# Performance work log

Measured on AMD Instinct MI355X. Metric: run time of the kernel, lower is better.

Reference implementation:

```python
import jax, jax.numpy as jnp
import numpy as np

WS = 7        # window size
NH = 8        # num heads


def setup_inputs() -> dict:
    key = jax.random.key(0)
    ks = jax.random.split(key, 5)
    B, N, C = 32, 3136, 512
    x = jax.random.normal(ks[0], (B, N, C), dtype=jnp.float32)
    s = 1.0 / np.sqrt(C)
    w_qkv = jax.random.normal(ks[1], (C, 3 * C), dtype=jnp.float32) * s
    b_qkv = jax.random.normal(ks[2], (3 * C,), dtype=jnp.float32) * 0.01
    w_proj = jax.random.normal(ks[3], (C, C), dtype=jnp.float32) * s
    b_proj = jax.random.normal(ks[4], (C,), dtype=jnp.float32) * 0.01
    return {"x": x, "w_qkv": w_qkv, "b_qkv": b_qkv, "w_proj": w_proj, "b_proj": b_proj}


def reference(x, w_qkv, b_qkv, w_proj, b_proj):
    B, N, C = x.shape
    H = W = int(round(N ** 0.5))
    hd = C // NH
    t = WS * WS  # 49 tokens per window
    # window partition: (B,N,C) -> (nW, 49, C)
    xw = x.reshape(B, H // WS, WS, W // WS, WS, C)
    xw = jnp.transpose(xw, (0, 1, 3, 2, 4, 5)).reshape(-1, t, C)
    # qkv projection; NOTE: no head permute (faithful to source), so
    # q,k,v : (nW, 49, NH, hd)
    qkv = (xw @ w_qkv + b_qkv).reshape(-1, t, 3, NH, hd)
    q, k, v = qkv[:, :, 0], qkv[:, :, 1], qkv[:, :, 2]
    # q @ k^T contracts head_dim, attends over heads axis: (nW, 49, NH, NH)
    attn = jnp.einsum('wthd,wtgd->wthg', q, k) * (hd ** -0.5)
    attn = jax.nn.softmax(attn, axis=-1)
    out = jnp.einsum('wthg,wtgd->wthd', attn, v)          # (nW, 49, NH, hd)
    # faithful transpose(1,2).reshape(-1, 49, C) (scrambles layout, as in torch)
    out = jnp.transpose(out, (0, 2, 1, 3)).reshape(-1, t, C)
    out = out @ w_proj + b_proj
    # window merge back to (B, N, C)
    out = out.reshape(B, H // WS, W // WS, WS, WS, C)
    out = jnp.transpose(out, (0, 1, 3, 2, 4, 5)).reshape(B, N, C)
    return out
```

## Files before the change

### kernel.cpp

```cpp
#include <hip/hip_runtime.h>
#include <stdint.h>
#include <stddef.h>

typedef short s16;
typedef __attribute__((ext_vector_type(8))) short short8;
typedef __attribute__((ext_vector_type(4))) float floatx4;

__device__ __forceinline__ float bf2f(short s) {
    union { float f; uint32_t u; } c; c.u = ((uint32_t)(uint16_t)s) << 16; return c.f;
}
__device__ __forceinline__ short f2bf(float f) {
    union { float f; uint32_t u; } c; c.f = f;
    uint32_t u = c.u;
    u += 0x7fffu + ((u >> 16) & 1u);
    return (short)(u >> 16);
}

__global__ __launch_bounds__(256) void cvt_kernel(const float* __restrict__ src,
                                                  s16* __restrict__ dst) {
    size_t i = (size_t)blockIdx.x * 256 + threadIdx.x;
    const floatx4* s4 = (const floatx4*)src;
    floatx4 a = s4[i * 2], b = s4[i * 2 + 1];
    short8 o;
    o[0] = f2bf(a[0]); o[1] = f2bf(a[1]); o[2] = f2bf(a[2]); o[3] = f2bf(a[3]);
    o[4] = f2bf(b[0]); o[5] = f2bf(b[1]); o[6] = f2bf(b[2]); o[7] = f2bf(b[3]);
    ((short8*)dst)[i] = o;
}

__global__ __launch_bounds__(256) void transpose_kernel(const float* __restrict__ w,
                                                        s16* __restrict__ wt,
                                                        int K, int N) {
    int idx = blockIdx.x * 256 + threadIdx.x;
    if (idx >= K * N) return;
    int n = idx / K, k = idx - n * K;
    wt[idx] = f2bf(w[(size_t)k * N + n]);
}

__device__ __forceinline__ const s16* x_row_ptr(const s16* xb, int m) {
    int win = m / 49, t = m - win * 49;
    int b = win >> 6, rem = win & 63, hb = rem >> 3, wb = rem & 7;
    int r = t / 7, c = t - r * 7;
    int n = (hb * 7 + r) * 56 + wb * 7 + c;
    return xb + ((size_t)b * 3136 + n) * 512;
}

template <int MODE>
__global__ __launch_bounds__(256) void gemm_kernel(const s16* __restrict__ A,
                                                   const s16* __restrict__ Bt,
                                                   const float* __restrict__ bias,
                                                   void* __restrict__ outp) {
    constexpr int NT = (MODE == 0) ? 12 : 4;
    const int tm = blockIdx.x / NT, tn = blockIdx.x % NT;
    const int tid = threadIdx.x, wave = tid >> 6, lane = tid & 63;

    __shared__ s16 lA[128 * 64];
    __shared__ s16 lB[128 * 64];

    const int sub  = lane >> 3;
    const int col8 = (((lane & 7) ^ sub) << 3);
    const s16* a_src[4];
    const s16* b_src[4];
#pragma unroll
    for (int i = 0; i < 4; ++i) {
        int ch = wave * 4 + i;
        int row = ch * 8 + sub;
        if (MODE == 0) a_src[i] = x_row_ptr(A, tm * 128 + row) + col8;
        else           a_src[i] = A + (size_t)(tm * 128 + row) * 512 + col8;
        b_src[i] = Bt + (size_t)(tn * 128 + row) * 512 + col8;
    }

    floatx4 acc[4][4];
#pragma unroll
    for (int mt = 0; mt < 4; ++mt)
#pragma unroll
        for (int nt = 0; nt < 4; ++nt)
            acc[mt][nt] = (floatx4){0.f, 0.f, 0.f, 0.f};

    const int wm = wave >> 1, wn = wave & 1;
    const int lm = lane & 15, quad = lane >> 4;

    for (int kt = 0; kt < 8; ++kt) {
#pragma unroll
        for (int i = 0; i < 4; ++i) {
            int ch = wave * 4 + i;
            __builtin_amdgcn_global_load_lds(
                (const __attribute__((address_space(1))) void*)a_src[i],
                (__attribute__((address_space(3))) void*)&lA[ch * 512], 16, 0, 0);
            __builtin_amdgcn_global_load_lds(
                (const __attribute__((address_space(1))) void*)b_src[i],
                (__attribute__((address_space(3))) void*)&lB[ch * 512], 16, 0, 0);
            a_src[i] += 64;
            b_src[i] += 64;
        }
        __syncthreads();
#pragma unroll
        for (int kb = 0; kb < 2; ++kb) {
            const int cb = kb * 4 + quad;
            const int sw = (cb ^ (lm & 7)) << 3;
            short8 af[4], bq[4];
#pragma unroll
            for (int mt = 0; mt < 4; ++mt)
                af[mt] = *(const short8*)&lA[(wm * 64 + mt * 16 + lm) * 64 + sw];
#pragma unroll
            for (int nt = 0; nt < 4; ++nt)
                bq[nt] = *(const short8*)&lB[(wn * 64 + nt * 16 + lm) * 64 + sw];
#pragma unroll
            for (int mt = 0; mt < 4; ++mt)
#pragma unroll
                for (int nt = 0; nt < 4; ++nt)
                    acc[mt][nt] = __builtin_amdgcn_mfma_f32_16x16x32_bf16(
                        af[mt], bq[nt], acc[mt][nt], 0, 0, 0);
        }
        __syncthreads();
    }

    float bv[4];
#pragma unroll
    for (int nt = 0; nt < 4; ++nt)
        bv[nt] = bias[tn * 128 + wn * 64 + nt * 16 + lm];

#pragma unroll
    for (int mt = 0; mt < 4; ++mt) {
        int mbase = tm * 128 + wm * 64 + mt * 16 + quad * 4;
#pragma unroll
        for (int i = 0; i < 4; ++i) {
            int m = mbase + i;
            size_t rowoff;
            if (MODE == 1) {
                int win = m / 49, t = m - win * 49;
                int b = win >> 6, rem = win & 63, hb = rem >> 3, wb = rem & 7;
                int r = t / 7, c = t - r * 7;
                int n = (hb * 7 + r) * 56 + wb * 7 + c;
                rowoff = ((size_t)b * 3136 + n) * 512;
            } else {
                rowoff = (size_t)m * 1536;
            }
#pragma unroll
            for (int nt = 0; nt < 4; ++nt) {
                int coln = tn * 128 + wn * 64 + nt * 16 + lm;
                float v = acc[mt][nt][i] + bv[nt];
                if (MODE == 0) ((s16*)outp)[rowoff + coln] = f2bf(v);
                else           ((float*)outp)[rowoff + coln] = v;
            }
        }
    }
}

__global__ __launch_bounds__(256) void attn_kernel(const s16* __restrict__ qkv,
                                                   s16* __restrict__ attn) {
    const int tid = threadIdx.x, wave = tid >> 6, lane = tid & 63;
    const int m = blockIdx.x * 4 + wave;

    __shared__ s16 sh[4][1536];
    s16* my = sh[wave];
    const s16* row = qkv + (size_t)m * 1536;
#pragma unroll
    for (int i = 0; i < 3; ++i)
        *(short8*)&my[i * 512 + lane * 8] = *(const short8*)&row[i * 512 + lane * 8];
    __syncthreads();

    const int h = lane >> 3, g = lane & 7;
    const s16* qs = my + h * 64;
    const s16* ks = my + 512 + g * 64;
    const s16* vs = my + 1024;

    float s = 0.f;
#pragma unroll
    for (int db = 0; db < 8; ++db) {
        int d0 = ((db + h) & 7) * 8;
        short8 q8 = *(const short8*)&qs[d0];
        short8 k8 = *(const short8*)&ks[d0];
#pragma unroll
        for (int j = 0; j < 8; ++j) s += bf2f(q8[j]) * bf2f(k8[j]);
    }
    s *= 0.125f;

    float mx = s;
    mx = fmaxf(mx, __shfl_xor(mx, 1));
    mx = fmaxf(mx, __shfl_xor(mx, 2));
    mx = fmaxf(mx, __shfl_xor(mx, 4));
    float p = __expf(s - mx);
    float sum = p;
    sum += __shfl_xor(sum, 1);
    sum += __shfl_xor(sum, 2);
    sum += __shfl_xor(sum, 4);
    p /= sum;

    float o[8];
#pragma unroll
    for (int j = 0; j < 8; ++j) o[j] = 0.f;
    const int dgrp = (lane & 7) * 8;
#pragma unroll
    for (int gg = 0; gg < 8; ++gg) {
        float pg = __shfl(p, h * 8 + gg);
        short8 v8 = *(const short8*)&vs[gg * 64 + dgrp];
#pragma unroll
        for (int j = 0; j < 8; ++j) o[j] += pg * bf2f(v8[j]);
    }

    int win = m / 49, t = m - win * 49;
    s16* dst = attn + (size_t)win * 25088 + h * 3136 + t * 64 + dgrp;
    short8 ob;
#pragma unroll
    for (int j = 0; j < 8; ++j) ob[j] = f2bf(o[j]);
    *(short8*)dst = ob;
}

extern "C" void kernel_launch(void* const* d_in, const int* in_sizes, int n_in,
                              void* d_out, int out_size, void* d_ws, size_t ws_size,
                              hipStream_t stream) {
    const float* x      = (const float*)d_in[0];
    const float* w_qkv  = (const float*)d_in[1];
    const float* b_qkv  = (const float*)d_in[2];
    const float* w_proj = (const float*)d_in[3];
    const float* b_proj = (const float*)d_in[4];

    char* ws = (char*)d_ws;
    s16* xbf    = (s16*)ws;
    s16* qkv    = (s16*)(ws + 102760448ull);
    s16* attn   = (s16*)(ws + 102760448ull + 308281344ull);
    s16* wqkvT  = (s16*)(ws + 102760448ull + 308281344ull + 102760448ull);
    s16* wprojT = (s16*)(ws + 102760448ull + 308281344ull + 102760448ull + 1572864ull);

    cvt_kernel<<<25088, 256, 0, stream>>>(x, xbf);
    transpose_kernel<<<3072, 256, 0, stream>>>(w_qkv, wqkvT, 512, 1536);
    transpose_kernel<<<1024, 256, 0, stream>>>(w_proj, wprojT, 512, 512);
    gemm_kernel<0><<<784 * 12, 256, 0, stream>>>(xbf, wqkvT, b_qkv, qkv);
    attn_kernel<<<25088, 256, 0, stream>>>(qkv, attn);
    gemm_kernel<1><<<784 * 4, 256, 0, stream>>>(attn, wprojT, b_proj, d_out);
}
```

Baseline: 812.4 us.

## Triple-buffer GEMM LDS loads with 256x128 tiles, 8 waves, XCD-aware block remap

Restructures both GEMM kernels to use 512-thread blocks computing 256x128 tiles, with a three-stage LDS ring so global-to-LDS copies for k-steps ahead overlap MFMA work. The per-iteration double __syncthreads is replaced by one vmcnt wait plus barrier. A block-index swizzle spreads consecutive tiles across the 8 XCDs, and setprio raises priority around the MFMA burst. It aims to hide memory latency and improve B-tile reuse, at the cost of 144KB of shared memory, which limits occupancy.

```diff
diff --git a/kernel.cpp b/kernel.cpp
--- a/kernel.cpp
+++ b/kernel.cpp
@@ -45,29 +45,56 @@
 }
 
 template <int MODE>
-__global__ __launch_bounds__(256) void gemm_kernel(const s16* __restrict__ A,
-                                                   const s16* __restrict__ Bt,
-                                                   const float* __restrict__ bias,
-                                                   void* __restrict__ outp) {
-    constexpr int NT = (MODE == 0) ? 12 : 4;
-    const int tm = blockIdx.x / NT, tn = blockIdx.x % NT;
+__global__ __launch_bounds__(512, 2) void gemm_kernel(const s16* __restrict__ A,
+                                                      const s16* __restrict__ Bt,
+                                                      const float* __restrict__ bias,
+                                                      void* __restrict__ outp) {
+    constexpr int NT  = (MODE == 0) ? 12 : 4;
+    constexpr int CPX = (MODE == 0) ? 588 : 196;
+
+    const int o  = (blockIdx.x & 7) * CPX + (blockIdx.x >> 3);
+    const int tm = o / NT, tn = o - tm * NT;
+
     const int tid = threadIdx.x, wave = tid >> 6, lane = tid & 63;
 
-    __shared__ s16 lA[128 * 64];
-    __shared__ s16 lB[128 * 64];
+    __shared__ s16 lA[3][256 * 64];
+    __shared__ s16 lB[3][128 * 64];
 
     const int sub  = lane >> 3;
     const int col8 = (((lane & 7) ^ sub) << 3);
     const s16* a_src[4];
-    const s16* b_src[4];
+    const s16* b_src[2];
 #pragma unroll
     for (int i = 0; i < 4; ++i) {
-        int ch = wave * 4 + i;
-        int row = ch * 8 + sub;
-        if (MODE == 0) a_src[i] = x_row_ptr(A, tm * 128 + row) + col8;
-        else           a_src[i] = A + (size_t)(tm * 128 + row) * 512 + col8;
+        int row = (wave * 4 + i) * 8 + sub;
+        if (MODE == 0) a_src[i] = x_row_ptr(A, tm * 256 + row) + col8;
+        else           a_src[i] = A + (size_t)(tm * 256 + row) * 512 + col8;
+    }
+#pragma unroll
+    for (int i = 0; i < 2; ++i) {
+        int row = (wave * 2 + i) * 8 + sub;
         b_src[i] = Bt + (size_t)(tn * 128 + row) * 512 + col8;
     }
+
+#define STAGE(buf)                                                              \
+    do {                                                                        \
+        _Pragma("unroll")                                                       \
+        for (int i_ = 0; i_ < 4; ++i_) {                                        \
+            __builtin_amdgcn_global_load_lds(                                   \
+                (const __attribute__((address_space(1))) void*)a_src[i_],       \
+                (__attribute__((address_space(3))) void*)&lA[buf][(wave * 4 + i_) * 512], \
+                16, 0, 0);                                                      \
+            a_src[i_] += 64;                                                    \
+        }                                                                       \
+        _Pragma("unroll")                                                       \
+        for (int i_ = 0; i_ < 2; ++i_) {                                        \
+            __builtin_amdgcn_global_load_lds(                                   \
+                (const __attribute__((address_space(1))) void*)b_src[i_],       \
+                (__attribute__((address_space(3))) void*)&lB[buf][(wave * 2 + i_) * 512], \
+                16, 0, 0);                                                      \
+            b_src[i_] += 64;                                                    \
+        }                                                                       \
+    } while (0)
 
     floatx4 acc[4][4];
 #pragma unroll
@@ -79,40 +106,48 @@
     const int wm = wave >> 1, wn = wave & 1;
     const int lm = lane & 15, quad = lane >> 4;
 
+    STAGE(0);
+    STAGE(1);
+    asm volatile("s_waitcnt vmcnt(6)" ::: "memory");
+    __builtin_amdgcn_s_barrier();
+    __builtin_amdgcn_sched_barrier(0);
+
+#pragma unroll
     for (int kt = 0; kt < 8; ++kt) {
-#pragma unroll
-        for (int i = 0; i < 4; ++i) {
-            int ch = wave * 4 + i;
-            __builtin_amdgcn_global_load_lds(
-                (const __attribute__((address_space(1))) void*)a_src[i],
-                (__attribute__((address_space(3))) void*)&lA[ch * 512], 16, 0, 0);
-            __builtin_amdgcn_global_load_lds(
-                (const __attribute__((address_space(1))) void*)b_src[i],
-                (__attribute__((address_space(3))) void*)&lB[ch * 512], 16, 0, 0);
-            a_src[i] += 64;
-            b_src[i] += 64;
+        if (kt + 2 < 8) STAGE((kt + 2) % 3);
+        const int cur = kt % 3;
+
+        short8 af[4][2], bq[4][2];
+#pragma unroll
+        for (int kk = 0; kk < 2; ++kk) {
+            const int sw = (((kk << 2) | quad) ^ (lm & 7)) << 3;
+#pragma unroll
+            for (int mt = 0; mt < 4; ++mt)
+                af[mt][kk] = *(const short8*)&lA[cur][(wm * 64 + mt * 16 + lm) * 64 + sw];
+#pragma unroll
+            for (int nt = 0; nt < 4; ++nt)
+                bq[nt][kk] = *(const short8*)&lB[cur][(wn * 64 + nt * 16 + lm) * 64 + sw];
         }
-        __syncthreads();
-#pragma unroll
-        for (int kb = 0; kb < 2; ++kb) {
-            const int cb = kb * 4 + quad;
-            const int sw = (cb ^ (lm & 7)) << 3;
-            short8 af[4], bq[4];
-#pragma unroll
-            for (int mt = 0; mt < 4; ++mt)
-                af[mt] = *(const short8*)&lA[(wm * 64 + mt * 16 + lm) * 64 + sw];
-#pragma unroll
-            for (int nt = 0; nt < 4; ++nt)
-                bq[nt] = *(const short8*)&lB[(wn * 64 + nt * 16 + lm) * 64 + sw];
+
+        __builtin_amdgcn_s_setprio(1);
+#pragma unroll
+        for (int kk = 0; kk < 2; ++kk)
 #pragma unroll
             for (int mt = 0; mt < 4; ++mt)
 #pragma unroll
                 for (int nt = 0; nt < 4; ++nt)
                     acc[mt][nt] = __builtin_amdgcn_mfma_f32_16x16x32_bf16(
-                        af[mt], bq[nt], acc[mt][nt], 0, 0, 0);
+                        af[mt][kk], bq[nt][kk], acc[mt][nt], 0, 0, 0);
+        __builtin_amdgcn_s_setprio(0);
+
+        if (kt < 7) {
+            if (kt < 6) asm volatile("s_waitcnt vmcnt(6)" ::: "memory");
+            else        asm volatile("s_waitcnt vmcnt(0)" ::: "memory");
+            __builtin_amdgcn_s_barrier();
+            __builtin_amdgcn_sched_barrier(0);
         }
-        __syncthreads();
-    }
+    }
+#undef STAGE
 
     float bv[4];
 #pragma unroll
@@ -121,7 +156,7 @@
 
 #pragma unroll
     for (int mt = 0; mt < 4; ++mt) {
-        int mbase = tm * 128 + wm * 64 + mt * 16 + quad * 4;
+        int mbase = tm * 256 + wm * 64 + mt * 16 + quad * 4;
 #pragma unroll
         for (int i = 0; i < 4; ++i) {
             int m = mbase + i;
@@ -225,7 +260,7 @@
     cvt_kernel<<<25088, 256, 0, stream>>>(x, xbf);
     transpose_kernel<<<3072, 256, 0, stream>>>(w_qkv, wqkvT, 512, 1536);
     transpose_kernel<<<1024, 256, 0, stream>>>(w_proj, wprojT, 512, 512);
-    gemm_kernel<0><<<784 * 12, 256, 0, stream>>>(xbf, wqkvT, b_qkv, qkv);
+    gemm_kernel<0><<<392 * 12, 512, 0, stream>>>(xbf, wqkvT, b_qkv, qkv);
     attn_kernel<<<25088, 256, 0, stream>>>(qkv, attn);
-    gemm_kernel<1><<<784 * 4, 256, 0, stream>>>(attn, wprojT, b_proj, d_out);
-}
+    gemm_kernel<1><<<392 * 4, 512, 0, stream>>>(attn, wprojT, b_proj, d_out);
+}
```

Measured after the change: 833.2 us. 1.03x slower.
